# Performance work log

Measured on AMD Instinct MI355X. Metric: run time of the kernel, lower is better.

## Reference

```python
import jax, jax.numpy as jnp
import numpy as np

N_ANG, N_EL, N_SAMP, NZ, NX = 8, 128, 2048, 384, 192
DEPTH_M = 0.04  # max one-way path length in meters


def setup_inputs() -> dict:
    key = jax.random.key(0)
    k0, k1, k2, k3, k4 = jax.random.split(key, 5)
    rf = jax.random.normal(k0, (N_ANG, N_EL, N_SAMP), jnp.float32)
    t0 = jax.random.uniform(k1, (N_ANG,), jnp.float32) * 1e-6
    d_tx = jax.random.uniform(k2, (N_ANG, NZ, NX), jnp.float32) * DEPTH_M
    d_rx = jax.random.uniform(k3, (N_EL, NZ, NX), jnp.float32) * DEPTH_M
    apod = jax.random.uniform(k4, (N_EL, NZ, NX), jnp.float32)
    fs = jnp.float32(20e6)    # 20 MHz sampling rate
    c0 = jnp.float32(1540.0)  # speed of sound in tissue, m/s
    return {"rf": rf, "t0": t0, "d_tx": d_tx, "d_rx": d_rx,
            "fs": fs, "c0": c0, "apod": apod}


def reference(rf, t0, d_tx, d_rx, fs, c0, apod):
    n_angles, n_elements, n_samples = rf.shape
    _, nz, nx = d_tx.shape
    # two-way delay per (angle, element, pixel): [A, E, nz, nx]
    tau = t0[:, None, None, None] + (d_tx[:, None, :, :] + d_rx[None, :, :, :]) / c0
    s_idx = jnp.clip(tau * fs, 0.0, float(n_samples - 1.001))
    idx_low = jnp.floor(s_idx).astype(jnp.int32)        # max n_samples-2
    idx_frac = s_idx - idx_low.astype(s_idx.dtype)
    flat_low = idx_low.reshape(n_angles, n_elements, nz * nx)
    s_low = jnp.take_along_axis(rf, flat_low, axis=2).reshape(n_angles, n_elements, nz, nx)
    s_high = jnp.take_along_axis(rf, flat_low + 1, axis=2).reshape(n_angles, n_elements, nz, nx)
    sampled = s_low + idx_frac * (s_high - s_low)       # linear interp
    return jnp.sum(sampled * apod[None], axis=1)        # reduce over elements -> [A, nz, nx]
```

## Files before the change

kernel.cpp:

```cpp
#include <hip/hip_runtime.h>


#define N_ANG 8
#define N_EL 128
#define N_SAMP 2048
#define NPIX (384*192)
#define WIN 1152
#define TPB 256
#define TILE 1024
#define PPT (TILE/TPB)
#define NTILE (NPIX/TILE)
#define NCHUNK 8
#define EPC (N_EL/NCHUNK)

__global__ __launch_bounds__(TPB, 4)
void das_partial(const float* __restrict__ rf, const float* __restrict__ t0,
                 const float* __restrict__ d_tx, const float* __restrict__ d_rx,
                 const float* __restrict__ fsp, const float* __restrict__ c0p,
                 const float* __restrict__ apod, float* __restrict__ part,
                 float* __restrict__ out, int use_atomic)
{
    __shared__ __align__(16) float smem[N_ANG * WIN];
    const int tid   = threadIdx.x;
    const int chunk = blockIdx.x / NTILE;
    const int tile  = blockIdx.x % NTILE;
    const int pbase = tile * TILE;
    const float fs    = fsp[0];
    const float scale = fs / c0p[0];

    float P[N_ANG][PPT], acc[N_ANG][PPT];
    #pragma unroll
    for (int a = 0; a < N_ANG; ++a) {
        const float t0fs = t0[a] * fs;
        #pragma unroll
        for (int k = 0; k < PPT; ++k) {
            P[a][k] = t0fs + d_tx[(size_t)a*NPIX + pbase + k*TPB + tid] * scale;
            acc[a][k] = 0.f;
        }
    }

    for (int i = 0; i < EPC; ++i) {
        const int e = chunk*EPC + i;

        float drxs[PPT], ap[PPT];
        #pragma unroll
        for (int k = 0; k < PPT; ++k) {
            const size_t off = (size_t)e*NPIX + pbase + k*TPB + tid;
            drxs[k] = d_rx[off] * scale;
            ap[k]   = apod[off];
        }

        #pragma unroll 3
        for (int r = 0; r < 9; ++r) {
            const int f = r*(TPB*4) + tid*4;
            const int a = f / WIN;
            const int s = f - a*WIN;
            *reinterpret_cast<float4*>(&smem[f]) =
                *reinterpret_cast<const float4*>(&rf[(size_t)(a*N_EL + e)*N_SAMP + s]);
        }

        __syncthreads();

        #pragma unroll
        for (int a = 0; a < N_ANG; ++a) {
            const float* row = &smem[a*WIN];
            #pragma unroll
            for (int k = 0; k < PPT; ++k) {
                const float sx = P[a][k] + drxs[k];
                const float fl = floorf(sx);
                const int   il = (int)fl;
                const float fr = sx - fl;
                const float lo = row[il];
                const float hi = row[il + 1];
                const float t  = __builtin_fmaf(-fr, lo, lo);
                const float r2 = __builtin_fmaf( fr, hi, t);
                acc[a][k] = __builtin_fmaf(ap[k], r2, acc[a][k]);
            }
        }

        __syncthreads();
    }

    if (!use_atomic) {
        #pragma unroll
        for (int a = 0; a < N_ANG; ++a)
            #pragma unroll
            for (int k = 0; k < PPT; ++k)
                part[(size_t)(chunk*N_ANG + a)*NPIX + pbase + k*TPB + tid] = acc[a][k];
    } else {
        #pragma unroll
        for (int a = 0; a < N_ANG; ++a)
            #pragma unroll
            for (int k = 0; k < PPT; ++k)
                atomicAdd(&out[(size_t)a*NPIX + pbase + k*TPB + tid], acc[a][k]);
    }
}

__global__ void das_reduce(const float* __restrict__ part, float* __restrict__ out)
{
    const int i = blockIdx.x * TPB + threadIdx.x;
    float s = 0.f;
    #pragma unroll
    for (int ch = 0; ch < NCHUNK; ++ch)
        s += part[(size_t)ch * (N_ANG*NPIX) + i];
    out[i] = s;
}

extern "C" void kernel_launch(void* const* d_in, const int* in_sizes, int n_in,
                              void* d_out, int out_size, void* d_ws, size_t ws_size,
                              hipStream_t stream)
{
    const float* rf   = (const float*)d_in[0];
    const float* t0   = (const float*)d_in[1];
    const float* dtx  = (const float*)d_in[2];
    const float* drx  = (const float*)d_in[3];
    const float* fs   = (const float*)d_in[4];
    const float* c0   = (const float*)d_in[5];
    const float* apod = (const float*)d_in[6];
    float* out = (float*)d_out;

    const size_t part_bytes = (size_t)NCHUNK * N_ANG * NPIX * sizeof(float);
    if (ws_size >= part_bytes) {
        das_partial<<<NCHUNK*NTILE, TPB, 0, stream>>>(rf, t0, dtx, drx, fs, c0, apod,
                                                      (float*)d_ws, out, 0);
        das_reduce<<<(N_ANG*NPIX)/TPB, TPB, 0, stream>>>((const float*)d_ws, out);
    } else {
        hipMemsetAsync(d_out, 0, (size_t)N_ANG*NPIX*sizeof(float), stream);
        das_partial<<<NCHUNK*NTILE, TPB, 0, stream>>>(rf, t0, dtx, drx, fs, c0, apod,
                                                      nullptr, out, 1);
    }
}
```

Measured before the change: 163.7 us.

## Double-buffer RF window in shared memory and prefetch next element's data

Adds a two-slot shared-memory buffer and register prefetch, so the next element's RF window, d_rx and apod loads are issued before the current element's interpolation runs. They are stored to LDS afterwards, and one barrier per iteration is dropped. It also halves the pixel tile to 512 per block, doubling the block count, and lowers launch bounds occupancy to 2 to make room for the extra registers and shared memory. The risks are lower occupancy, higher register pressure from the 9 float4 staging registers, and twice the LDS per block.

```diff
diff --git a/kernel.cpp b/kernel.cpp
--- a/kernel.cpp
+++ b/kernel.cpp
@@ -7,26 +7,27 @@
 #define NPIX (384*192)
 #define WIN 1152
 #define TPB 256
-#define TILE 1024
+#define TILE 512
 #define PPT (TILE/TPB)
 #define NTILE (NPIX/TILE)
 #define NCHUNK 8
 #define EPC (N_EL/NCHUNK)
 
-__global__ __launch_bounds__(TPB, 4)
+__global__ __launch_bounds__(TPB, 2)
 void das_partial(const float* __restrict__ rf, const float* __restrict__ t0,
                  const float* __restrict__ d_tx, const float* __restrict__ d_rx,
                  const float* __restrict__ fsp, const float* __restrict__ c0p,
                  const float* __restrict__ apod, float* __restrict__ part,
                  float* __restrict__ out, int use_atomic)
 {
-    __shared__ __align__(16) float smem[N_ANG * WIN];
+    __shared__ __align__(16) float smem[2][N_ANG * WIN];
     const int tid   = threadIdx.x;
     const int chunk = blockIdx.x / NTILE;
     const int tile  = blockIdx.x % NTILE;
     const int pbase = tile * TILE;
     const float fs    = fsp[0];
     const float scale = fs / c0p[0];
+    const int e0 = chunk * EPC;
 
     float P[N_ANG][PPT], acc[N_ANG][PPT];
     #pragma unroll
@@ -39,31 +40,50 @@
         }
     }
 
+    float drxs[PPT], ap[PPT];
+    #pragma unroll
+    for (int k = 0; k < PPT; ++k) {
+        const size_t off = (size_t)e0*NPIX + pbase + k*TPB + tid;
+        drxs[k] = d_rx[off] * scale;
+        ap[k]   = apod[off];
+    }
+    #pragma unroll
+    for (int r = 0; r < 9; ++r) {
+        const int f = r*(TPB*4) + tid*4;
+        const int a = f / WIN;
+        const int s = f - a*WIN;
+        *reinterpret_cast<float4*>(&smem[0][f]) =
+            *reinterpret_cast<const float4*>(&rf[(size_t)(a*N_EL + e0)*N_SAMP + s]);
+    }
+    __syncthreads();
+
+    #pragma unroll 2
     for (int i = 0; i < EPC; ++i) {
-        const int e = chunk*EPC + i;
+        const bool more = (i + 1 < EPC);
 
-        float drxs[PPT], ap[PPT];
-        #pragma unroll
-        for (int k = 0; k < PPT; ++k) {
-            const size_t off = (size_t)e*NPIX + pbase + k*TPB + tid;
-            drxs[k] = d_rx[off] * scale;
-            ap[k]   = apod[off];
+        float4 st[9];
+        float dr2[PPT], ap2[PPT];
+        if (more) {
+            const int en = e0 + i + 1;
+            #pragma unroll
+            for (int r = 0; r < 9; ++r) {
+                const int f = r*(TPB*4) + tid*4;
+                const int a = f / WIN;
+                const int s = f - a*WIN;
+                st[r] = *reinterpret_cast<const float4*>(&rf[(size_t)(a*N_EL + en)*N_SAMP + s]);
+            }
+            #pragma unroll
+            for (int k = 0; k < PPT; ++k) {
+                const size_t off = (size_t)en*NPIX + pbase + k*TPB + tid;
+                dr2[k] = d_rx[off] * scale;
+                ap2[k] = apod[off];
+            }
         }
 
-        #pragma unroll 3
-        for (int r = 0; r < 9; ++r) {
-            const int f = r*(TPB*4) + tid*4;
-            const int a = f / WIN;
-            const int s = f - a*WIN;
-            *reinterpret_cast<float4*>(&smem[f]) =
-                *reinterpret_cast<const float4*>(&rf[(size_t)(a*N_EL + e)*N_SAMP + s]);
-        }
-
-        __syncthreads();
-
+        const float* buf = smem[i & 1];
         #pragma unroll
         for (int a = 0; a < N_ANG; ++a) {
-            const float* row = &smem[a*WIN];
+            const float* row = &buf[a*WIN];
             #pragma unroll
             for (int k = 0; k < PPT; ++k) {
                 const float sx = P[a][k] + drxs[k];
@@ -78,6 +98,18 @@
             }
         }
 
+        if (more) {
+            #pragma unroll
+            for (int r = 0; r < 9; ++r) {
+                const int f = r*(TPB*4) + tid*4;
+                *reinterpret_cast<float4*>(&smem[(i + 1) & 1][f]) = st[r];
+            }
+            #pragma unroll
+            for (int k = 0; k < PPT; ++k) {
+                drxs[k] = dr2[k];
+                ap[k]   = ap2[k];
+            }
+        }
         __syncthreads();
     }
 
```

After: 330.5 us. 2.02x slower.
